# Performance work log

Measured on AMD Instinct MI355X. Metric: run time of the kernel, lower is better.

Reference implementation:

```python
import jax, jax.numpy as jnp
import numpy as np
from jax import lax

NQ = 8          # num_qubits
NL = 2          # q_layers
SCALE_RANGE = 0.5

# sign table for <Z_i>: Z[i, s] = +1 if bit i of basis state s is 0 else -1
_BITS = ((np.arange(2 ** NQ)[None, :] >> (NQ - 1 - np.arange(NQ))[:, None]) & 1)
_ZSIGN = np.asarray(1.0 - 2.0 * _BITS, np.float32)  # [NQ, 2**NQ]


def _apply_1q(state, U, wire):
    # state: (2,)*NQ complex, U: [2,2]
    s = jnp.tensordot(U, state, axes=[[1], [wire]])
    return jnp.moveaxis(s, 0, wire)


def _apply_cnot(state, c, t):
    G = jnp.array([[1, 0, 0, 0], [0, 1, 0, 0], [0, 0, 0, 1], [0, 0, 1, 0]],
                  dtype=state.dtype).reshape(2, 2, 2, 2)
    s = jnp.tensordot(G, state, axes=[[2, 3], [c, t]])
    return jnp.moveaxis(s, [0, 1], [c, t])


def _ry(t):
    c, s = jnp.cos(t / 2), jnp.sin(t / 2)
    return jnp.stack([jnp.stack([c, -s]), jnp.stack([s, c])]).astype(jnp.complex64)


def _rz(t):
    e = jnp.exp(-0.5j * t.astype(jnp.complex64))
    z = jnp.zeros((), jnp.complex64)
    return jnp.stack([jnp.stack([e, z]), jnp.stack([z, jnp.conj(e)])])


def _rot(phi, theta, omega):
    # PennyLane Rot(phi, theta, omega) = RZ(omega) @ RY(theta) @ RZ(phi)
    return _rz(omega) @ _ry(theta) @ _rz(phi)


def _circuit(angles, weights):
    # angles: [NQ], weights: [NL, NQ, 3] -> expvals [NQ]
    state = jnp.zeros((2,) * NQ, jnp.complex64).at[(0,) * NQ].set(1.0)
    # AngleEmbedding (rotation='Y')
    for i in range(NQ):
        state = _apply_1q(state, _ry(angles[i]), i)
    # StronglyEntanglingLayers (default ranges)
    for l in range(NL):
        for i in range(NQ):
            state = _apply_1q(state, _rot(weights[l, i, 0], weights[l, i, 1], weights[l, i, 2]), i)
        r = (l % (NQ - 1)) + 1
        for i in range(NQ):
            state = _apply_cnot(state, i, (i + r) % NQ)
    probs = jnp.abs(state.reshape(-1)) ** 2          # [2**NQ]
    return jnp.asarray(_ZSIGN) @ probs               # [NQ] expvals of PauliZ


def _forward(q, k, v, W_angles, b_angles, q_weights, W_post, b_post):
    B, n_heads, T, head_dim = q.shape
    # summary [B, H] from q (mean over T); torch code detaches it -> stop_gradient
    summary = q.transpose(0, 2, 1, 3).reshape(B, T, n_heads * head_dim).mean(axis=1)
    summary = lax.stop_gradient(summary)
    # to_angles under no_grad; circuit uses q_weights.detach()
    angles = lax.stop_gradient(summary @ W_angles.T + b_angles)        # [B, NQ]
    qfeat = lax.stop_gradient(jax.vmap(lambda a: _circuit(a, q_weights))(angles))  # [B, NQ]
    head_logits = qfeat @ W_post.T + b_post                            # [B, n_heads]
    scales = 1.0 + SCALE_RANGE * jnp.tanh(head_logits)
    sb = scales.astype(q.dtype).reshape(B, n_heads, 1, 1)  # per-head scale
    return q * sb, k * sb, v * sb


def setup_inputs() -> dict:
    key = jax.random.key(0)
    ks = jax.random.split(key, 8)
    B, NH, T, HD = 32, 16, 1024, 64
    H = NH * HD
    return {
        "q": jax.random.normal(ks[0], (B, NH, T, HD), jnp.float32),
        "k": jax.random.normal(ks[1], (B, NH, T, HD), jnp.float32),
        "v": jax.random.normal(ks[2], (B, NH, T, HD), jnp.float32),
        "W_angles": jax.random.normal(ks[3], (NQ, H), jnp.float32) * 0.02,
        "b_angles": jax.random.normal(ks[4], (NQ,), jnp.float32) * 0.02,
        "q_weights": jax.random.normal(ks[5], (NL, NQ, 3), jnp.float32) * 0.01,
        "W_post": jax.random.normal(ks[6], (NH, NQ), jnp.float32) * 0.1,
        "b_post": jax.random.normal(ks[7], (NH,), jnp.float32) * 0.1,
    }


def reference(q, k, v, W_angles, b_angles, q_weights, W_post, b_post):
    return _forward(q, k, v, W_angles, b_angles, q_weights, W_post, b_post)
```

## Files before the change

### kernel.cpp

```cpp
#include <hip/hip_runtime.h>
#include <math.h>

#define NQ 8
#define NSTATES 256
#define BB 32
#define NH 16
#define TT 1024
#define HD 64
#define HH 1024
#define NCHUNK 8

typedef float f32x4 __attribute__((ext_vector_type(4)));

__global__ __launch_bounds__(256) void k_summary(const f32x4* __restrict__ q4,
                                                 float* __restrict__ part) {
    const int blk   = blockIdx.x;
    const int bid   = blk >> 3;
    const int chunk = blk & 7;
    const int t     = threadIdx.x;
    const int hd4   = t & 15;
    const int tg    = t >> 4;
    const f32x4* base = q4 + (size_t)bid * (TT * (HD / 4))
                           + (size_t)chunk * 128 * (HD / 4);

    f32x4 acc = (f32x4)(0.f);
#pragma unroll
    for (int i = 0; i < 8; ++i) {
        acc += base[(tg + 16 * i) * (HD / 4) + hd4];
    }

    __shared__ f32x4 red[256];
    red[t] = acc;
    __syncthreads();
    for (int s = 8; s > 0; s >>= 1) {
        if (tg < s) red[t] += red[t + s * 16];
        __syncthreads();
    }
    if (tg == 0) {
        f32x4 r = red[t];
        float* out = part + (size_t)blk * HD + hd4 * 4;
        out[0] = r.x; out[1] = r.y; out[2] = r.z; out[3] = r.w;
    }
}

__global__ __launch_bounds__(256) void k_circuit(
        const float* __restrict__ part, const float* __restrict__ W_angles,
        const float* __restrict__ b_angles, const float* __restrict__ q_weights,
        const float* __restrict__ W_post, const float* __restrict__ b_post,
        float* __restrict__ scales) {
    const int b = blockIdx.x;
    const int t = threadIdx.x;

    __shared__ float  ssum[HH];
    __shared__ float  ang[NQ];
    __shared__ float2 st[NSTATES];
    __shared__ float  zred[4][NQ];
    __shared__ float  qfeat[NQ];

    for (int h = t; h < HH; h += 256) {
        const int nh = h >> 6, hd = h & 63;
        const float* p = part + ((size_t)(b * NH + nh) * NCHUNK) * HD + hd;
        float s = 0.f;
#pragma unroll
        for (int c = 0; c < NCHUNK; ++c) s += p[c * HD];
        ssum[h] = s * (1.0f / (float)TT);
    }
    __syncthreads();

    {
        const int i = t >> 5;
        const int j = t & 31;
        const float* wrow = W_angles + i * HH;
        float p = 0.f;
        for (int h = j; h < HH; h += 32) p += ssum[h] * wrow[h];
        for (int off = 16; off; off >>= 1) p += __shfl_xor(p, off);
        if (j == 0) ang[i] = p + b_angles[i];
    }

    st[t] = make_float2(t == 0 ? 1.f : 0.f, 0.f);
    __syncthreads();

    auto gate1q = [&](int wire, float2 M00, float2 M01, float2 M10, float2 M11) {
        const int m = 1 << (7 - wire);
        float2 a0 = st[t & ~m];
        float2 a1 = st[t |  m];
        __syncthreads();
        float2 r;
        if (t & m) {
            r.x = M10.x * a0.x - M10.y * a0.y + M11.x * a1.x - M11.y * a1.y;
            r.y = M10.x * a0.y + M10.y * a0.x + M11.x * a1.y + M11.y * a1.x;
        } else {
            r.x = M00.x * a0.x - M00.y * a0.y + M01.x * a1.x - M01.y * a1.y;
            r.y = M00.x * a0.y + M00.y * a0.x + M01.x * a1.y + M01.y * a1.x;
        }
        st[t] = r;
        __syncthreads();
    };

    auto cnot = [&](int cw, int tw) {
        const int cm = 1 << (7 - cw);
        const int tm = 1 << (7 - tw);
        float2 a = st[(t & cm) ? (t ^ tm) : t];
        __syncthreads();
        st[t] = a;
        __syncthreads();
    };

    for (int i = 0; i < NQ; ++i) {
        const float half = 0.5f * ang[i];
        const float c = cosf(half), s = sinf(half);
        gate1q(i, make_float2(c, 0.f), make_float2(-s, 0.f),
                  make_float2(s, 0.f), make_float2(c, 0.f));
    }

    for (int l = 0; l < 2; ++l) {
        for (int i = 0; i < NQ; ++i) {
            const float phi = q_weights[(l * NQ + i) * 3 + 0];
            const float th  = q_weights[(l * NQ + i) * 3 + 1];
            const float om  = q_weights[(l * NQ + i) * 3 + 2];
            const float c = cosf(0.5f * th), s = sinf(0.5f * th);
            const float apo = -0.5f * (phi + om);
            const float amo =  0.5f * (phi - om);
            float2 M00 = make_float2( c * cosf(apo),  c * sinf(apo));
            float2 M11 = make_float2( c * cosf(apo), -c * sinf(apo));
            float2 M01 = make_float2(-s * cosf(amo), -s * sinf(amo));
            float2 M10 = make_float2( s * cosf(amo), -s * sinf(amo));
            gate1q(i, M00, M01, M10, M11);
        }
        const int r = (l % (NQ - 1)) + 1;
        for (int i = 0; i < NQ; ++i) cnot(i, (i + r) % NQ);
    }

    {
        float2 a = st[t];
        float p = a.x * a.x + a.y * a.y;
        float z[NQ];
        for (int i = 0; i < NQ; ++i)
            z[i] = ((t >> (7 - i)) & 1) ? -p : p;
        for (int off = 32; off; off >>= 1)
            for (int i = 0; i < NQ; ++i) z[i] += __shfl_xor(z[i], off);
        const int wid = t >> 6, lane = t & 63;
        if (lane == 0)
            for (int i = 0; i < NQ; ++i) zred[wid][i] = z[i];
        __syncthreads();
        if (t < NQ) qfeat[t] = zred[0][t] + zred[1][t] + zred[2][t] + zred[3][t];
        __syncthreads();
    }

    if (t < NH) {
        float lg = b_post[t];
        for (int i = 0; i < NQ; ++i) lg += qfeat[i] * W_post[t * NQ + i];
        scales[b * NH + t] = 1.0f + 0.5f * tanhf(lg);
    }
}

__global__ __launch_bounds__(256) void k_scale(
        const f32x4* __restrict__ q4, const f32x4* __restrict__ k4,
        const f32x4* __restrict__ v4, const float* __restrict__ scales,
        f32x4* __restrict__ out4) {
    const int  perTensor = BB * NH * TT * HD / 4;
    const int  tens = blockIdx.y;
    const int  blk  = blockIdx.x;
    const int  t    = threadIdx.x;
    const float s   = scales[blk >> 4];

    const f32x4* in = (tens == 0) ? q4 : (tens == 1) ? k4 : v4;
    const size_t base = (size_t)blk * 1024;
    const f32x4* inp  = in + base;
    f32x4*       outp = out4 + (size_t)tens * perTensor + base;

#pragma unroll
    for (int i = 0; i < 4; ++i) {
        const int idx = i * 256 + t;
        f32x4 x = (tens == 0) ? inp[idx]
                              : __builtin_nontemporal_load(&inp[idx]);
        x *= s;
        __builtin_nontemporal_store(x, &outp[idx]);
    }
}

extern "C" void kernel_launch(void* const* d_in, const int* in_sizes, int n_in,
                              void* d_out, int out_size, void* d_ws, size_t ws_size,
                              hipStream_t stream) {
    const float* q        = (const float*)d_in[0];
    const float* k        = (const float*)d_in[1];
    const float* v        = (const float*)d_in[2];
    const float* W_angles = (const float*)d_in[3];
    const float* b_ang    = (const float*)d_in[4];
    const float* q_w      = (const float*)d_in[5];
    const float* W_post   = (const float*)d_in[6];
    const float* b_post   = (const float*)d_in[7];
    float* out = (float*)d_out;

    float* part   = (float*)d_ws;
    float* scales = part + (size_t)BB * NH * NCHUNK * HD;

    k_summary<<<BB * NH * NCHUNK, 256, 0, stream>>>((const f32x4*)q, part);
    k_circuit<<<BB, 256, 0, stream>>>(part, W_angles, b_ang, q_w,
                                      W_post, b_post, scales);
    dim3 grid(8192, 3);
    k_scale<<<grid, 256, 0, stream>>>((const f32x4*)q, (const f32x4*)k,
                                      (const f32x4*)v, scales, (f32x4*)out);
}
```

Baseline: 187.7 us.

## Run circuit simulation in one wavefront with register amplitudes and shuffles

The quantum circuit kernel now runs on a single 64-lane wavefront, with each lane holding 4 amplitudes in registers. Gates on the two high wires are applied inside each lane, and the other wires use cross-lane shuffles, which removes the shared-memory state and the many block barriers per gate. The summary and angle projection are also computed per lane with shuffle reductions. Separately, the scale kernel now handles twice as many elements per block with half as many blocks.

New measurement: 191.5 us. 1.02x slower.

```diff
diff --git a/kernel.cpp b/kernel.cpp
--- a/kernel.cpp
+++ b/kernel.cpp
@@ -2,7 +2,6 @@
 #include <math.h>
 
 #define NQ 8
-#define NSTATES 256
 #define BB 32
 #define NH 16
 #define TT 1024
@@ -43,81 +42,131 @@
     }
 }
 
-__global__ __launch_bounds__(256) void k_circuit(
+__global__ __launch_bounds__(64) void k_circuit(
         const float* __restrict__ part, const float* __restrict__ W_angles,
         const float* __restrict__ b_angles, const float* __restrict__ q_weights,
         const float* __restrict__ W_post, const float* __restrict__ b_post,
         float* __restrict__ scales) {
     const int b = blockIdx.x;
-    const int t = threadIdx.x;
-
-    __shared__ float  ssum[HH];
-    __shared__ float  ang[NQ];
-    __shared__ float2 st[NSTATES];
-    __shared__ float  zred[4][NQ];
-    __shared__ float  qfeat[NQ];
-
-    for (int h = t; h < HH; h += 256) {
-        const int nh = h >> 6, hd = h & 63;
-        const float* p = part + ((size_t)(b * NH + nh) * NCHUNK) * HD + hd;
+    const int l = threadIdx.x;
+
+    float sm[16];
+    const float* pb = part + (size_t)b * NH * NCHUNK * HD;
+#pragma unroll
+    for (int m = 0; m < 16; ++m) {
+        const float* p = pb + (size_t)m * NCHUNK * HD + l;
         float s = 0.f;
 #pragma unroll
         for (int c = 0; c < NCHUNK; ++c) s += p[c * HD];
-        ssum[h] = s * (1.0f / (float)TT);
-    }
-    __syncthreads();
-
-    {
-        const int i = t >> 5;
-        const int j = t & 31;
-        const float* wrow = W_angles + i * HH;
-        float p = 0.f;
-        for (int h = j; h < HH; h += 32) p += ssum[h] * wrow[h];
-        for (int off = 16; off; off >>= 1) p += __shfl_xor(p, off);
-        if (j == 0) ang[i] = p + b_angles[i];
-    }
-
-    st[t] = make_float2(t == 0 ? 1.f : 0.f, 0.f);
-    __syncthreads();
+        sm[m] = s * (1.0f / (float)TT);
+    }
+
+    float ang[NQ];
+#pragma unroll
+    for (int i = 0; i < NQ; ++i) {
+        const float* w = W_angles + i * HH;
+        float d = 0.f;
+#pragma unroll
+        for (int m = 0; m < 16; ++m) d += sm[m] * w[m * 64 + l];
+#pragma unroll
+        for (int off = 32; off; off >>= 1) d += __shfl_xor(d, off);
+        ang[i] = d + b_angles[i];
+    }
+
+    float2 amp[4];
+    amp[0] = make_float2(l == 0 ? 1.f : 0.f, 0.f);
+    amp[1] = amp[2] = amp[3] = make_float2(0.f, 0.f);
+
+    auto cmul_add2 = [](float2 A, float2 v, float2 B, float2 w) {
+        float2 r;
+        r.x = A.x * v.x - A.y * v.y + B.x * w.x - B.y * w.y;
+        r.y = A.x * v.y + A.y * v.x + B.x * w.y + B.y * w.x;
+        return r;
+    };
 
     auto gate1q = [&](int wire, float2 M00, float2 M01, float2 M10, float2 M11) {
-        const int m = 1 << (7 - wire);
-        float2 a0 = st[t & ~m];
-        float2 a1 = st[t |  m];
-        __syncthreads();
-        float2 r;
-        if (t & m) {
-            r.x = M10.x * a0.x - M10.y * a0.y + M11.x * a1.x - M11.y * a1.y;
-            r.y = M10.x * a0.y + M10.y * a0.x + M11.x * a1.y + M11.y * a1.x;
+        if (wire < 2) {
+            const int rm = (wire == 0) ? 2 : 1;
+#pragma unroll
+            for (int r = 0; r < 4; ++r) {
+                if (!(r & rm)) {
+                    float2 a0 = amp[r], a1 = amp[r | rm];
+                    amp[r]      = cmul_add2(M00, a0, M01, a1);
+                    amp[r | rm] = cmul_add2(M10, a0, M11, a1);
+                }
+            }
         } else {
-            r.x = M00.x * a0.x - M00.y * a0.y + M01.x * a1.x - M01.y * a1.y;
-            r.y = M00.x * a0.y + M00.y * a0.x + M01.x * a1.y + M01.y * a1.x;
+            const int m = 1 << (7 - wire);
+#pragma unroll
+            for (int r = 0; r < 4; ++r) {
+                float2 o;
+                o.x = __shfl_xor(amp[r].x, m);
+                o.y = __shfl_xor(amp[r].y, m);
+                const bool hi = (l & m) != 0;
+                float2 a0 = hi ? o : amp[r];
+                float2 a1 = hi ? amp[r] : o;
+                amp[r] = hi ? cmul_add2(M10, a0, M11, a1)
+                            : cmul_add2(M00, a0, M01, a1);
+            }
         }
-        st[t] = r;
-        __syncthreads();
     };
 
-    auto cnot = [&](int cw, int tw) {
-        const int cm = 1 << (7 - cw);
-        const int tm = 1 << (7 - tw);
-        float2 a = st[(t & cm) ? (t ^ tm) : t];
-        __syncthreads();
-        st[t] = a;
-        __syncthreads();
+    auto cnot = [&](int c, int t) {
+        const bool creg = (c < 2), treg = (t < 2);
+        if (creg && treg) {
+            if (c == 0) { float2 tmp = amp[2]; amp[2] = amp[3]; amp[3] = tmp; }
+            else        { float2 tmp = amp[1]; amp[1] = amp[3]; amp[3] = tmp; }
+        } else if (creg && !treg) {
+            const int tm = 1 << (7 - t);
+#pragma unroll
+            for (int r = 0; r < 4; ++r) {
+                float2 o;
+                o.x = __shfl_xor(amp[r].x, tm);
+                o.y = __shfl_xor(amp[r].y, tm);
+                const bool sel = (c == 0) ? ((r & 2) != 0) : ((r & 1) != 0);
+                if (sel) amp[r] = o;
+            }
+        } else if (!creg && treg) {
+            const int cm = 1 << (7 - c);
+            const bool ctl = (l & cm) != 0;
+            if (t == 0) {
+                float2 a = amp[0], bq = amp[2];
+                amp[0] = ctl ? bq : a;  amp[2] = ctl ? a : bq;
+                float2 cq = amp[1], d = amp[3];
+                amp[1] = ctl ? d : cq;  amp[3] = ctl ? cq : d;
+            } else {
+                float2 a = amp[0], bq = amp[1];
+                amp[0] = ctl ? bq : a;  amp[1] = ctl ? a : bq;
+                float2 cq = amp[2], d = amp[3];
+                amp[2] = ctl ? d : cq;  amp[3] = ctl ? cq : d;
+            }
+        } else {
+            const int cm = 1 << (7 - c), tm = 1 << (7 - t);
+            const bool ctl = (l & cm) != 0;
+#pragma unroll
+            for (int r = 0; r < 4; ++r) {
+                float2 o;
+                o.x = __shfl_xor(amp[r].x, tm);
+                o.y = __shfl_xor(amp[r].y, tm);
+                if (ctl) amp[r] = o;
+            }
+        }
     };
 
+#pragma unroll
     for (int i = 0; i < NQ; ++i) {
-        const float half = 0.5f * ang[i];
-        const float c = cosf(half), s = sinf(half);
+        const float c = cosf(0.5f * ang[i]), s = sinf(0.5f * ang[i]);
         gate1q(i, make_float2(c, 0.f), make_float2(-s, 0.f),
                   make_float2(s, 0.f), make_float2(c, 0.f));
     }
 
-    for (int l = 0; l < 2; ++l) {
+#pragma unroll
+    for (int lay = 0; lay < 2; ++lay) {
+#pragma unroll
         for (int i = 0; i < NQ; ++i) {
-            const float phi = q_weights[(l * NQ + i) * 3 + 0];
-            const float th  = q_weights[(l * NQ + i) * 3 + 1];
-            const float om  = q_weights[(l * NQ + i) * 3 + 2];
+            const float phi = q_weights[(lay * NQ + i) * 3 + 0];
+            const float th  = q_weights[(lay * NQ + i) * 3 + 1];
+            const float om  = q_weights[(lay * NQ + i) * 3 + 2];
             const float c = cosf(0.5f * th), s = sinf(0.5f * th);
             const float apo = -0.5f * (phi + om);
             const float amo =  0.5f * (phi - om);
@@ -127,30 +176,32 @@
             float2 M10 = make_float2( s * cosf(amo), -s * sinf(amo));
             gate1q(i, M00, M01, M10, M11);
         }
-        const int r = (l % (NQ - 1)) + 1;
-        for (int i = 0; i < NQ; ++i) cnot(i, (i + r) % NQ);
-    }
-
-    {
-        float2 a = st[t];
-        float p = a.x * a.x + a.y * a.y;
-        float z[NQ];
-        for (int i = 0; i < NQ; ++i)
-            z[i] = ((t >> (7 - i)) & 1) ? -p : p;
-        for (int off = 32; off; off >>= 1)
-            for (int i = 0; i < NQ; ++i) z[i] += __shfl_xor(z[i], off);
-        const int wid = t >> 6, lane = t & 63;
-        if (lane == 0)
-            for (int i = 0; i < NQ; ++i) zred[wid][i] = z[i];
-        __syncthreads();
-        if (t < NQ) qfeat[t] = zred[0][t] + zred[1][t] + zred[2][t] + zred[3][t];
-        __syncthreads();
-    }
-
-    if (t < NH) {
-        float lg = b_post[t];
-        for (int i = 0; i < NQ; ++i) lg += qfeat[i] * W_post[t * NQ + i];
-        scales[b * NH + t] = 1.0f + 0.5f * tanhf(lg);
+        const int r = lay + 1;
+#pragma unroll
+        for (int i = 0; i < NQ; ++i) cnot(i, (i + r) & 7);
+    }
+
+    const float p0 = amp[0].x * amp[0].x + amp[0].y * amp[0].y;
+    const float p1 = amp[1].x * amp[1].x + amp[1].y * amp[1].y;
+    const float p2 = amp[2].x * amp[2].x + amp[2].y * amp[2].y;
+    const float p3 = amp[3].x * amp[3].x + amp[3].y * amp[3].y;
+    const float pl = p0 + p1 + p2 + p3;
+    float z[NQ];
+    z[0] = (p0 + p1) - (p2 + p3);
+    z[1] = (p0 + p2) - (p1 + p3);
+#pragma unroll
+    for (int i = 2; i < NQ; ++i)
+        z[i] = ((l >> (7 - i)) & 1) ? -pl : pl;
+#pragma unroll
+    for (int off = 32; off; off >>= 1)
+#pragma unroll
+        for (int i = 0; i < NQ; ++i) z[i] += __shfl_xor(z[i], off);
+
+    if (l < NH) {
+        float lg = b_post[l];
+#pragma unroll
+        for (int i = 0; i < NQ; ++i) lg += z[i] * W_post[l * NQ + i];
+        scales[b * NH + l] = 1.0f + 0.5f * tanhf(lg);
     }
 }
 
@@ -162,15 +213,15 @@
     const int  tens = blockIdx.y;
     const int  blk  = blockIdx.x;
     const int  t    = threadIdx.x;
-    const float s   = scales[blk >> 4];
+    const float s   = scales[blk >> 3];
 
     const f32x4* in = (tens == 0) ? q4 : (tens == 1) ? k4 : v4;
-    const size_t base = (size_t)blk * 1024;
+    const size_t base = (size_t)blk * 2048;
     const f32x4* inp  = in + base;
     f32x4*       outp = out4 + (size_t)tens * perTensor + base;
 
 #pragma unroll
-    for (int i = 0; i < 4; ++i) {
+    for (int i = 0; i < 8; ++i) {
         const int idx = i * 256 + t;
         f32x4 x = (tens == 0) ? inp[idx]
                               : __builtin_nontemporal_load(&inp[idx]);
@@ -196,9 +247,9 @@
     float* scales = part + (size_t)BB * NH * NCHUNK * HD;
 
     k_summary<<<BB * NH * NCHUNK, 256, 0, stream>>>((const f32x4*)q, part);
-    k_circuit<<<BB, 256, 0, stream>>>(part, W_angles, b_ang, q_w,
-                                      W_post, b_post, scales);
-    dim3 grid(8192, 3);
+    k_circuit<<<BB, 64, 0, stream>>>(part, W_angles, b_ang, q_w,
+                                     W_post, b_post, scales);
+    dim3 grid(4096, 3);
     k_scale<<<grid, 256, 0, stream>>>((const f32x4*)q, (const f32x4*)k,
                                       (const f32x4*)v, scales, (f32x4*)out);
 }
```
